# Performance work log

Hardware: AMD Instinct MI355X
Metric: run time of the kernel (lower is better)

The kernel has to match this reference:

```python
import jax, jax.numpy as jnp
import numpy as np

B = 4_194_304
N_LAYERS = 2


def setup_inputs() -> dict:
    key = jax.random.key(0)
    k1, k2 = jax.random.split(key)
    x = jax.random.normal(k1, (B, 2), dtype=jnp.float32)
    q_weights = 0.01 * jax.random.normal(k2, (N_LAYERS, 2), dtype=jnp.float32)
    return {"x": x, "q_weights": q_weights}


def _apply_rx(state, theta, qubit):
    """Apply RX(theta) to `qubit` of a batched 2-qubit state [B,2,2].
    RX(t) = [[cos(t/2), -i sin(t/2)], [-i sin(t/2), cos(t/2)]].
    theta: [B] (per-sample) or scalar (shared weight)."""
    b = state.shape[0]
    theta = jnp.broadcast_to(theta, (b,))
    c = jnp.cos(0.5 * theta)[:, None].astype(state.dtype)
    s = (-1j * jnp.sin(0.5 * theta))[:, None].astype(state.dtype)
    if qubit == 0:
        a0, a1 = state[:, 0, :], state[:, 1, :]
        return jnp.stack([c * a0 + s * a1, s * a0 + c * a1], axis=1)
    else:
        a0, a1 = state[:, :, 0], state[:, :, 1]
        return jnp.stack([c * a0 + s * a1, s * a0 + c * a1], axis=2)


def _cnot01(state):
    # control = qubit0, target = qubit1: swap target amps where control == 1
    return jnp.stack([state[:, 0, :], state[:, 1, ::-1]], axis=1)


def reference(x, q_weights):
    b = x.shape[0]
    # |00> initial state, batched: [B, 2, 2] (axes = qubit0, qubit1)
    state = jnp.zeros((b, 2, 2), dtype=jnp.complex64).at[:, 0, 0].set(1.0)
    # AngleEmbedding (default rotation = RX) with per-sample angles
    state = _apply_rx(state, x[:, 0], 0)
    state = _apply_rx(state, x[:, 1], 1)
    # BasicEntanglerLayers: per layer RX on each wire, then single CNOT(0,1)
    for l in range(q_weights.shape[0]):
        state = _apply_rx(state, q_weights[l, 0], 0)
        state = _apply_rx(state, q_weights[l, 1], 1)
        state = _cnot01(state)
    # <Z_0> = P(qubit0=0) - P(qubit0=1)
    probs = jnp.real(state * jnp.conj(state))
    expz0 = jnp.sum(probs[:, 0, :], axis=-1) - jnp.sum(probs[:, 1, :], axis=-1)
    return (0.5 * (expz0 + 1.0)).astype(jnp.float32).reshape(-1, 1)
```

## Files before the change

### kernel.cpp

```cpp
#include <hip/hip_runtime.h>
#include <math.h>

#define N_LAYERS 2

typedef float vfloat4 __attribute__((ext_vector_type(4)));

__device__ __forceinline__ void rx_pair(float2& a, float2& b, float c, float s) {
    float2 na = make_float2(fmaf(c, a.x,  s * b.y), fmaf(c, a.y, -s * b.x));
    float2 nb = make_float2(fmaf(s, a.y,  c * b.x), fmaf(-s, a.x, c * b.y));
    a = na; b = nb;
}

__device__ void compute_K(const float* __restrict__ w, float* __restrict__ K) {
    float2 U[4][4];
    for (int j = 0; j < 4; ++j)
        for (int r = 0; r < 4; ++r)
            U[j][r] = make_float2(j == r ? 1.f : 0.f, 0.f);

    for (int l = 0; l < N_LAYERS; ++l) {
        float t0 = 0.5f * w[2 * l + 0];
        float t1 = 0.5f * w[2 * l + 1];
        float c0 = __cosf(t0), s0 = __sinf(t0);
        float c1 = __cosf(t1), s1 = __sinf(t1);
        for (int j = 0; j < 4; ++j) {
            rx_pair(U[j][0], U[j][2], c0, s0);
            rx_pair(U[j][1], U[j][3], c0, s0);
            rx_pair(U[j][0], U[j][1], c1, s1);
            rx_pair(U[j][2], U[j][3], c1, s1);
            float2 tmp = U[j][2]; U[j][2] = U[j][3]; U[j][3] = tmp;
        }
    }

    float Mre[4][4], Mim[4][4];
    for (int j = 0; j < 4; ++j)
        for (int k = 0; k < 4; ++k) {
            float re = 0.f, im = 0.f;
            for (int m = 0; m < 2; ++m) {
                re += U[j][m].x * U[k][m].x + U[j][m].y * U[k][m].y;
                im += U[j][m].x * U[k][m].y - U[j][m].y * U[k][m].x;
            }
            Mre[j][k] = re; Mim[j][k] = im;
        }

    float N00 = Mre[0][0], N11 = Mre[1][1], N22 = Mre[2][2], N33 = Mre[3][3];
    float N01 = Mim[0][1], N23 = Mim[2][3], N02 = Mim[0][2], N13 = Mim[1][3];
    float N03 = -Mre[0][3], N12 = Mre[1][2];

    K[0] = 0.25f * (N00 + N11 + N22 + N33);
    K[1] = 0.25f * (N00 - N11 + N22 - N33);
    K[2] = 0.50f * (N01 + N23);
    K[3] = 0.25f * (N00 + N11 - N22 - N33);
    K[4] = 0.25f * (N00 - N11 - N22 + N33);
    K[5] = 0.50f * (N01 - N23);
    K[6] = 0.50f * (N02 + N13);
    K[7] = 0.50f * (N02 - N13);
    K[8] = 0.50f * (N03 + N12);
}

__device__ __forceinline__ float qnet_eval1(float x0, float x1,
                                            float k0, float k1, float k2,
                                            float k3, float k4, float k5,
                                            float k6, float k7, float k8) {
    float X0 = __cosf(x0), S0 = __sinf(x0);
    float X1 = __cosf(x1), S1 = __sinf(x1);
    float t0 = fmaf(k2, S1, fmaf(k1, X1, k0));
    float t1 = fmaf(k5, S1, fmaf(k4, X1, k3));
    float t2 = fmaf(k8, S1, fmaf(k7, X1, k6));
    return fmaf(S0, t2, fmaf(X0, t1, t0));
}

__global__ __launch_bounds__(256) void qnet_fused_kernel(
    const float4* __restrict__ x, const float* __restrict__ w,
    vfloat4* __restrict__ out, int nthreads) {
    int i = blockIdx.x * blockDim.x + threadIdx.x;
    bool act = (i < nthreads);

    float4 xa, xb;
    if (act) {
        xa = x[2 * i + 0];
        xb = x[2 * i + 1];
    }

    __shared__ float Ks[9];
    if (threadIdx.x == 0) compute_K(w, Ks);
    __syncthreads();

    float k0 = Ks[0], k1 = Ks[1], k2 = Ks[2];
    float k3 = Ks[3], k4 = Ks[4], k5 = Ks[5];
    float k6 = Ks[6], k7 = Ks[7], k8 = Ks[8];

    if (act) {
        vfloat4 r;
        r.x = qnet_eval1(xa.x, xa.y, k0, k1, k2, k3, k4, k5, k6, k7, k8);
        r.y = qnet_eval1(xa.z, xa.w, k0, k1, k2, k3, k4, k5, k6, k7, k8);
        r.z = qnet_eval1(xb.x, xb.y, k0, k1, k2, k3, k4, k5, k6, k7, k8);
        r.w = qnet_eval1(xb.z, xb.w, k0, k1, k2, k3, k4, k5, k6, k7, k8);
        __builtin_nontemporal_store(r, &out[i]);
    }
}

extern "C" void kernel_launch(void* const* d_in, const int* in_sizes, int n_in,
                              void* d_out, int out_size, void* d_ws, size_t ws_size,
                              hipStream_t stream) {
    const float* x = (const float*)d_in[0];
    const float* w = (const float*)d_in[1];

    int nthreads = in_sizes[0] / 8;
    int blocks = (nthreads + 255) / 256;
    qnet_fused_kernel<<<blocks, 256, 0, stream>>>(
        (const float4*)x, w, (vfloat4*)d_out, nthreads);
}
```

Baseline: 77.30 us.

## Split coefficient precompute into separate kernel and double per-thread work

Moves the per-block serial computation of the nine expectation coefficients into a tiny prelaunch kernel that writes them to workspace, so the main kernel just loads them and needs no block-wide barrier. Each thread now processes eight samples (four float4 loads, two vector stores) instead of four, and uses combined sincos calls. The cost is an extra kernel launch and a dependency on workspace, plus fewer threads in flight.

```diff
diff --git a/kernel.cpp b/kernel.cpp
--- a/kernel.cpp
+++ b/kernel.cpp
@@ -57,45 +57,63 @@
     K[8] = 0.50f * (N03 + N12);
 }
 
+__global__ __launch_bounds__(64) void qnet_coef_kernel(const float* __restrict__ w,
+                                                       float* __restrict__ K) {
+    if (threadIdx.x == 0) {
+        float Kl[9];
+        compute_K(w, Kl);
+        #pragma unroll
+        for (int j = 0; j < 9; ++j) K[j] = Kl[j];
+    }
+}
+
 __device__ __forceinline__ float qnet_eval1(float x0, float x1,
                                             float k0, float k1, float k2,
                                             float k3, float k4, float k5,
                                             float k6, float k7, float k8) {
-    float X0 = __cosf(x0), S0 = __sinf(x0);
-    float X1 = __cosf(x1), S1 = __sinf(x1);
+    float X0, S0, X1, S1;
+    __sincosf(x0, &S0, &X0);
+    __sincosf(x1, &S1, &X1);
     float t0 = fmaf(k2, S1, fmaf(k1, X1, k0));
     float t1 = fmaf(k5, S1, fmaf(k4, X1, k3));
     float t2 = fmaf(k8, S1, fmaf(k7, X1, k6));
     return fmaf(S0, t2, fmaf(X0, t1, t0));
 }
 
-__global__ __launch_bounds__(256) void qnet_fused_kernel(
-    const float4* __restrict__ x, const float* __restrict__ w,
-    vfloat4* __restrict__ out, int nthreads) {
+__global__ __launch_bounds__(256, 4) void qnet_eval_kernel(
+    const float4* __restrict__ x, const float* __restrict__ Kg,
+    vfloat4* __restrict__ out, int nquads) {
+    const float k0 = Kg[0], k1 = Kg[1], k2 = Kg[2],
+                k3 = Kg[3], k4 = Kg[4], k5 = Kg[5],
+                k6 = Kg[6], k7 = Kg[7], k8 = Kg[8];
+
     int i = blockIdx.x * blockDim.x + threadIdx.x;
-    bool act = (i < nthreads);
-
-    float4 xa, xb;
-    if (act) {
-        xa = x[2 * i + 0];
-        xb = x[2 * i + 1];
-    }
-
-    __shared__ float Ks[9];
-    if (threadIdx.x == 0) compute_K(w, Ks);
-    __syncthreads();
-
-    float k0 = Ks[0], k1 = Ks[1], k2 = Ks[2];
-    float k3 = Ks[3], k4 = Ks[4], k5 = Ks[5];
-    float k6 = Ks[6], k7 = Ks[7], k8 = Ks[8];
-
-    if (act) {
-        vfloat4 r;
-        r.x = qnet_eval1(xa.x, xa.y, k0, k1, k2, k3, k4, k5, k6, k7, k8);
-        r.y = qnet_eval1(xa.z, xa.w, k0, k1, k2, k3, k4, k5, k6, k7, k8);
-        r.z = qnet_eval1(xb.x, xb.y, k0, k1, k2, k3, k4, k5, k6, k7, k8);
-        r.w = qnet_eval1(xb.z, xb.w, k0, k1, k2, k3, k4, k5, k6, k7, k8);
-        __builtin_nontemporal_store(r, &out[i]);
+    int q0 = 2 * i;
+    if (q0 + 1 < nquads) {
+        float4 xa = x[2 * q0 + 0];
+        float4 xb = x[2 * q0 + 1];
+        float4 xc = x[2 * q0 + 2];
+        float4 xd = x[2 * q0 + 3];
+        vfloat4 r0, r1;
+        r0.x = qnet_eval1(xa.x, xa.y, k0, k1, k2, k3, k4, k5, k6, k7, k8);
+        r0.y = qnet_eval1(xa.z, xa.w, k0, k1, k2, k3, k4, k5, k6, k7, k8);
+        r0.z = qnet_eval1(xb.x, xb.y, k0, k1, k2, k3, k4, k5, k6, k7, k8);
+        r0.w = qnet_eval1(xb.z, xb.w, k0, k1, k2, k3, k4, k5, k6, k7, k8);
+        r1.x = qnet_eval1(xc.x, xc.y, k0, k1, k2, k3, k4, k5, k6, k7, k8);
+        r1.y = qnet_eval1(xc.z, xc.w, k0, k1, k2, k3, k4, k5, k6, k7, k8);
+        r1.z = qnet_eval1(xd.x, xd.y, k0, k1, k2, k3, k4, k5, k6, k7, k8);
+        r1.w = qnet_eval1(xd.z, xd.w, k0, k1, k2, k3, k4, k5, k6, k7, k8);
+        __builtin_nontemporal_store(r0, &out[q0 + 0]);
+        __builtin_nontemporal_store(r1, &out[q0 + 1]);
+    } else if (q0 < nquads) {
+        float4 xa = x[2 * q0 + 0];
+        float4 xb = x[2 * q0 + 1];
+        vfloat4 r0;
+        r0.x = qnet_eval1(xa.x, xa.y, k0, k1, k2, k3, k4, k5, k6, k7, k8);
+        r0.y = qnet_eval1(xa.z, xa.w, k0, k1, k2, k3, k4, k5, k6, k7, k8);
+        r0.z = qnet_eval1(xb.x, xb.y, k0, k1, k2, k3, k4, k5, k6, k7, k8);
+        r0.w = qnet_eval1(xb.z, xb.w, k0, k1, k2, k3, k4, k5, k6, k7, k8);
+        __builtin_nontemporal_store(r0, &out[q0]);
     }
 }
 
@@ -104,9 +122,13 @@
                               hipStream_t stream) {
     const float* x = (const float*)d_in[0];
     const float* w = (const float*)d_in[1];
+    float* K = (float*)d_ws;
 
-    int nthreads = in_sizes[0] / 8;
+    qnet_coef_kernel<<<1, 64, 0, stream>>>(w, K);
+
+    int nquads = in_sizes[0] / 8;
+    int nthreads = (nquads + 1) / 2;
     int blocks = (nthreads + 255) / 256;
-    qnet_fused_kernel<<<blocks, 256, 0, stream>>>(
-        (const float4*)x, w, (vfloat4*)d_out, nthreads);
+    qnet_eval_kernel<<<blocks, 256, 0, stream>>>(
+        (const float4*)x, K, (vfloat4*)d_out, nquads);
 }
```

Result: slower. 80.08 us (+3.6%).
